# Optimization experiments

Measured on AMD Instinct MI355X. Metric: run time of the kernel, lower is better.

The kernel has to match this reference:

```python
import jax, jax.numpy as jnp
import numpy as np

N = 100_000      # n_nodes
E = 1_600_000    # n_edges (avg degree 16)
D_IN, D_H, D_OUT = 128, 128, 64
SIM_THRESH = 0.1


def setup_inputs() -> dict:
    key = jax.random.key(0)
    k = jax.random.split(key, 6)
    row = jax.random.randint(k[0], (E,), 0, N, dtype=jnp.int32)
    off = jax.random.randint(k[1], (E,), 1, N, dtype=jnp.int32)
    col = ((row + off) % N).astype(jnp.int32)  # guarantees no self-loops
    edge_index = jnp.stack([row, col], axis=0)
    x = jax.random.normal(k[2], (N, D_IN), dtype=jnp.float32)
    W1 = jax.random.normal(k[3], (D_IN, D_H), dtype=jnp.float32) / np.sqrt(D_IN)
    b1 = jnp.zeros((D_H,), jnp.float32)
    W2 = jax.random.normal(k[4], (D_H, D_OUT), dtype=jnp.float32) / np.sqrt(D_H)
    b2 = jnp.zeros((D_OUT,), jnp.float32)
    return {"x": x, "edge_index": edge_index, "W1": W1, "b1": b1, "W2": W2, "b2": b2}


def _att_coef(x, row, col, valid):
    """Edge-wise cosine-similarity attention (GNNGuard att_coef), fixed edge set.
    valid: bool [E] mask of edges still alive (pass-1 pruning).
    Returns per-edge weight w [E] (0 for pruned edges), per-node self-loop
    weight w_self [N], and the surviving-edge mask."""
    # cosine similarity per edge (never materialize NxN)
    xn = x / jnp.maximum(jnp.linalg.norm(x, axis=1, keepdims=True), 1e-12)
    sim = jnp.einsum('ed,ed->e', xn[row], xn[col])           # [E]
    sim = jnp.where(sim < SIM_THRESH, 0.0, sim)
    sim = jnp.where(valid, sim, 0.0)
    # L1 row normalization (segment reduce over destination rows)
    rowsum = jax.ops.segment_sum(sim, row, num_segments=N)   # [N]
    rs = rowsum[row]
    att = jnp.where(rs > 0, sim / jnp.where(rs > 0, rs, 1.0), 0.0)
    nz = att > 0                                             # edges kept by sparse matrix
    # degree-based self-loop weight: lam = 1/(deg+1)
    deg = jax.ops.segment_sum(nz.astype(x.dtype), row, num_segments=N)
    lam = 1.0 / (deg + 1.0)
    # exponentiate only stored (nonzero) entries, matching scipy sparse semantics
    w = jnp.where(nz, jnp.exp(att), 0.0)                     # [E]
    w_self = jnp.exp(lam)                                    # [N]
    return w, w_self, nz


def _gcn_conv(x, row, col, w, w_self, W, b):
    """GCNConv with given edge weights + self-loop weights, symmetric norm."""
    h = x @ W                                                # [N, d_out]
    deg = jax.ops.segment_sum(w, row, num_segments=N) + w_self
    dinv = jnp.where(deg > 0, jax.lax.rsqrt(deg), 0.0)       # deg^-1/2
    we = dinv[row] * w * dinv[col]                           # [E]
    agg = jax.ops.segment_sum(we[:, None] * h[col], row, num_segments=N)
    agg = agg + (w_self * dinv * dinv)[:, None] * h          # self-loop term
    return agg + b


def reference(x, edge_index, W1, b1, W2, b2):
    row, col = edge_index[0], edge_index[1]
    all_valid = jnp.ones((E,), dtype=bool)
    # attention pass 1 on raw features
    w1e, w1s, nz1 = _att_coef(x, row, col, all_valid)
    h = jax.nn.relu(_gcn_conv(x, row, col, w1e, w1s, W1, b1))
    # attention pass 2 on hidden features, restricted to surviving edges
    # (self-loops added in pass 1 are stripped again before re-normalization)
    w2e, w2s, _ = _att_coef(h, row, col, nz1)
    # dropout is identity at inference (training=False)
    out = _gcn_conv(h, row, col, w2e, w2s, W2, b2)
    return jax.nn.log_softmax(out, axis=1)
```

## Files before the change

kernel.cpp:

```cpp
#include <hip/hip_runtime.h>
#include <math.h>

#define SIM_THRESH 0.1f
#define Q_SCREEN_THRESH 0.085f

static __device__ __forceinline__ int dot4i8(int a, int b, int acc) {
#if __has_builtin(__builtin_amdgcn_sdot4)
  return __builtin_amdgcn_sdot4(a, b, acc, false);
#else
  const char4 av = *(const char4*)&a;
  const char4 bv = *(const char4*)&b;
  return acc + (int)av.x * bv.x + (int)av.y * bv.y + (int)av.z * bv.z + (int)av.w * bv.w;
#endif
}

__global__ void norms_q_kernel(const float* __restrict__ x, float* __restrict__ norm,
                               char* __restrict__ qn, int n) {
  int gid = blockIdx.x * blockDim.x + threadIdx.x;
  int r = gid >> 6, lane = gid & 63;
  if (r >= n) return;
  float2 v = ((const float2*)(x + (size_t)r * 128))[lane];
  float s = v.x * v.x + v.y * v.y;
#pragma unroll
  for (int o = 1; o < 64; o <<= 1) s += __shfl_xor(s, o);
  float nr = sqrtf(s);
  if (lane == 0) norm[r] = nr;
  float inv = 127.f / fmaxf(nr, 1e-12f);
  int qa = (int)rintf(v.x * inv);
  int qb = (int)rintf(v.y * inv);
  unsigned short packed = (unsigned short)((qa & 0xff) | ((qb & 0xff) << 8));
  *(unsigned short*)(qn + (size_t)r * 128 + lane * 2) = packed;
}

template <int DOUT>
__global__ void __launch_bounds__(256) gemm_kernel(const float* __restrict__ X,
                                                   const float* __restrict__ W,
                                                   float* __restrict__ out, int n) {
  constexpr int BM = 128, BK = 32;
  constexpr int TN = DOUT / 16;
  constexpr int XS = BK + 4;
  constexpr int WS = DOUT + 4;
  __shared__ float Xs[BM * XS];
  __shared__ float Ws[BK * WS];

  const int t = threadIdx.x;
  const int tx = t & 15;
  const int ty = t >> 4;
  const int base = blockIdx.x * BM;

  float acc[8][TN];
#pragma unroll
  for (int i = 0; i < 8; ++i)
#pragma unroll
    for (int j = 0; j < TN; ++j) acc[i][j] = 0.f;

  const int lr = t >> 3;
  const int lk4 = (t & 7) * 4;
  constexpr int F4R = DOUT / 4;
  constexpr int KSTEP = 256 / F4R;
  const int wc = t % F4R;
  const int wk0 = t / F4R;

  for (int kb = 0; kb < 128; kb += BK) {
    __syncthreads();
#pragma unroll
    for (int j = 0; j < 4; ++j) {
      int r = lr + 32 * j;
      int gr = base + r;
      float4 v = make_float4(0.f, 0.f, 0.f, 0.f);
      if (gr < n) v = *(const float4*)(X + (size_t)gr * 128 + kb + lk4);
      *(float4*)(Xs + r * XS + lk4) = v;
    }
#pragma unroll
    for (int k = wk0; k < BK; k += KSTEP) {
      float4 v = *(const float4*)(W + (size_t)(kb + k) * DOUT + wc * 4);
      *(float4*)(Ws + k * WS + wc * 4) = v;
    }
    __syncthreads();

#pragma unroll
    for (int k4 = 0; k4 < BK; k4 += 4) {
      float4 xf[8];
#pragma unroll
      for (int i = 0; i < 8; ++i) xf[i] = *(const float4*)(Xs + (ty + 16 * i) * XS + k4);
      float4 wf[4][TN / 4];
#pragma unroll
      for (int kk = 0; kk < 4; ++kk)
#pragma unroll
        for (int jj = 0; jj < TN / 4; ++jj)
          wf[kk][jj] = *(const float4*)(Ws + (k4 + kk) * WS + tx * TN + jj * 4);
#pragma unroll
      for (int i = 0; i < 8; ++i) {
        const float xk[4] = {xf[i].x, xf[i].y, xf[i].z, xf[i].w};
#pragma unroll
        for (int kk = 0; kk < 4; ++kk) {
#pragma unroll
          for (int jj = 0; jj < TN / 4; ++jj) {
            acc[i][jj * 4 + 0] = fmaf(xk[kk], wf[kk][jj].x, acc[i][jj * 4 + 0]);
            acc[i][jj * 4 + 1] = fmaf(xk[kk], wf[kk][jj].y, acc[i][jj * 4 + 1]);
            acc[i][jj * 4 + 2] = fmaf(xk[kk], wf[kk][jj].z, acc[i][jj * 4 + 2]);
            acc[i][jj * 4 + 3] = fmaf(xk[kk], wf[kk][jj].w, acc[i][jj * 4 + 3]);
          }
        }
      }
    }
  }

#pragma unroll
  for (int i = 0; i < 8; ++i) {
    int gr = base + ty + 16 * i;
    if (gr < n) {
#pragma unroll
      for (int jj = 0; jj < TN / 4; ++jj) {
        float4 v = make_float4(acc[i][jj * 4 + 0], acc[i][jj * 4 + 1], acc[i][jj * 4 + 2],
                               acc[i][jj * 4 + 3]);
        *(float4*)(out + (size_t)gr * DOUT + tx * TN + jj * 4) = v;
      }
    }
  }
}

__global__ void sim1_kernel(const char* __restrict__ qn, const float* __restrict__ x,
                            const float* __restrict__ norm, const int* __restrict__ row,
                            const int* __restrict__ col, float* __restrict__ sim,
                            int* __restrict__ cnt, int e) {
  int gid = blockIdx.x * blockDim.x + threadIdx.x;
  int p = gid >> 4, l = gid & 15;
  if (p >= e) return;
  int r = __builtin_nontemporal_load(row + p);
  int c = __builtin_nontemporal_load(col + p);
  int2 qa = *(const int2*)(qn + (size_t)r * 128 + l * 8);
  int2 qb = *(const int2*)(qn + (size_t)c * 128 + l * 8);
  int si = 0;
  si = dot4i8(qa.x, qb.x, si);
  si = dot4i8(qa.y, qb.y, si);
#pragma unroll
  for (int o = 1; o < 16; o <<= 1) si += __shfl_xor(si, o);
  float v = (float)si * (1.f / 16129.f);
  if (v > Q_SCREEN_THRESH) {
    const float4* fr = (const float4*)(x + (size_t)r * 128) + 2 * l;
    const float4* fc = (const float4*)(x + (size_t)c * 128) + 2 * l;
    float4 a0 = fr[0], a1 = fr[1], b0 = fc[0], b1 = fc[1];
    float t = a0.x * b0.x + a0.y * b0.y + a0.z * b0.z + a0.w * b0.w + a1.x * b1.x + a1.y * b1.y +
              a1.z * b1.z + a1.w * b1.w;
#pragma unroll
    for (int o = 1; o < 16; o <<= 1) t += __shfl_xor(t, o);
    float nr = fmaxf(norm[r], 1e-12f), nc = fmaxf(norm[c], 1e-12f);
    v = t / (nr * nc);
  } else {
    v = 0.f;
  }
  if (l == 0) {
    v = (v < SIM_THRESH) ? 0.f : v;
    __builtin_nontemporal_store(v, sim + p);
    if (v > 0.f) atomicAdd(&cnt[r], 1);
  }
}

__global__ void scan1_kernel(const int* __restrict__ cnt, int* __restrict__ excl,
                             int* __restrict__ bsum, int n) {
  __shared__ int sd[256];
  int t = threadIdx.x;
  int base = blockIdx.x * 1024 + t * 4;
  int v[4];
  int s = 0;
#pragma unroll
  for (int k = 0; k < 4; k++) {
    int idx = base + k;
    v[k] = (idx < n) ? cnt[idx] : 0;
    s += v[k];
  }
  sd[t] = s;
  __syncthreads();
  for (int off = 1; off < 256; off <<= 1) {
    int tmp = (t >= off) ? sd[t - off] : 0;
    __syncthreads();
    sd[t] += tmp;
    __syncthreads();
  }
  int ex = sd[t] - s;
#pragma unroll
  for (int k = 0; k < 4; k++) {
    int idx = base + k;
    if (idx < n) excl[idx] = ex;
    ex += v[k];
  }
  if (t == 255) bsum[blockIdx.x] = sd[255];
}

__global__ void scan2_kernel(int* __restrict__ bsum, int nb, int* __restrict__ total_out) {
  if (threadIdx.x == 0 && blockIdx.x == 0) {
    int acc = 0;
    for (int i = 0; i < nb; i++) {
      int v = bsum[i];
      bsum[i] = acc;
      acc += v;
    }
    *total_out = acc;
  }
}

__global__ void scan3_kernel(int* __restrict__ excl, const int* __restrict__ bsum, int n) {
  int i = blockIdx.x * 1024 + threadIdx.x;
  if (i < n) excl[i] += bsum[blockIdx.x];
}

__global__ void fillc_kernel(const int* __restrict__ row, const int* __restrict__ col,
                             const float* __restrict__ sim, const int* __restrict__ rp,
                             int* __restrict__ cur, int4* __restrict__ rec, int e) {
  int i = blockIdx.x * blockDim.x + threadIdx.x;
  if (i < e) {
    float s = __builtin_nontemporal_load(sim + i);
    if (s > 0.f) {
      int r = __builtin_nontemporal_load(row + i);
      int cc = __builtin_nontemporal_load(col + i);
      int p = rp[r] + atomicAdd(&cur[r], 1);
      int4 v;
      v.x = r;
      v.y = cc;
      v.z = __float_as_int(s);
      v.w = 0;
      rec[p] = v;
    }
  }
}

__global__ void row_att1_kernel(const int* __restrict__ rp, const int4* __restrict__ rec,
                                float* __restrict__ w, float* __restrict__ wself,
                                float* __restrict__ dinv, int n) {
  int r = blockIdx.x * blockDim.x + threadIdx.x;
  if (r >= n) return;
  int s0 = rp[r], s1 = rp[r + 1];
  float rs = 0.f;
  for (int p = s0; p < s1; p++) rs += __int_as_float(rec[p].z);
  float degw = 0.f;
  for (int p = s0; p < s1; p++) {
    float wv = expf(__int_as_float(rec[p].z) / rs);
    w[p] = wv;
    degw += wv;
  }
  float ws = expf(1.f / (float)(s1 - s0 + 1));
  degw += ws;
  wself[r] = ws;
  dinv[r] = 1.f / sqrtf(degw);
}

__global__ void agg_relu_norm_kernel(const float* __restrict__ hin, const int* __restrict__ rp,
                                     const int4* __restrict__ rec, const float* __restrict__ w,
                                     const float* __restrict__ wself,
                                     const float* __restrict__ dinv,
                                     const float* __restrict__ bias, float* __restrict__ hout,
                                     float* __restrict__ normout, int n) {
  int gid = blockIdx.x * blockDim.x + threadIdx.x;
  int r = gid >> 6, lane = gid & 63;
  if (r >= n) return;
  float di = dinv[r];
  float2 acc = {0.f, 0.f};
  int s0 = rp[r], s1 = rp[r + 1];
  for (int p = s0; p < s1; p++) {
    int c = rec[p].y;
    float we = di * w[p] * dinv[c];
    float2 hv = ((const float2*)(hin + (size_t)c * 128))[lane];
    acc.x = fmaf(we, hv.x, acc.x);
    acc.y = fmaf(we, hv.y, acc.y);
  }
  float self = wself[r] * di * di;
  float2 hr = ((const float2*)(hin + (size_t)r * 128))[lane];
  float2 bv = ((const float2*)bias)[lane];
  acc.x = fmaf(self, hr.x, acc.x) + bv.x;
  acc.y = fmaf(self, hr.y, acc.y) + bv.y;
  acc.x = fmaxf(acc.x, 0.f);
  acc.y = fmaxf(acc.y, 0.f);
  ((float2*)(hout + (size_t)r * 128))[lane] = acc;
  float s = acc.x * acc.x + acc.y * acc.y;
#pragma unroll
  for (int o = 1; o < 64; o <<= 1) s += __shfl_xor(s, o);
  if (lane == 0) normout[r] = sqrtf(s);
}

__global__ void sim2_kernel(const float* __restrict__ h, const float* __restrict__ norm,
                            const int4* __restrict__ rec, const int* __restrict__ nnz_p,
                            float* __restrict__ sim2) {
  int nnz = *nnz_p;
  int tid = blockIdx.x * blockDim.x + threadIdx.x;
  int ngroups = (gridDim.x * blockDim.x) >> 4;
  int g = tid >> 4, l = tid & 15;
  for (int p = g; p < nnz; p += ngroups) {
    int4 rv = rec[p];
    int r = rv.x, c = rv.y;
    const float4* fr = (const float4*)(h + (size_t)r * 128) + 2 * l;
    const float4* fc = (const float4*)(h + (size_t)c * 128) + 2 * l;
    float4 a0 = fr[0], a1 = fr[1], b0 = fc[0], b1 = fc[1];
    float s = a0.x * b0.x + a0.y * b0.y + a0.z * b0.z + a0.w * b0.w + a1.x * b1.x + a1.y * b1.y +
              a1.z * b1.z + a1.w * b1.w;
#pragma unroll
    for (int o = 1; o < 16; o <<= 1) s += __shfl_xor(s, o);
    if (l == 0) {
      float nr = fmaxf(norm[r], 1e-12f), nc = fmaxf(norm[c], 1e-12f);
      float v = s / (nr * nc);
      sim2[p] = (v < SIM_THRESH) ? 0.f : v;
    }
  }
}

__global__ void row_att2_kernel(const int* __restrict__ rp, const float* __restrict__ sim2,
                                float* __restrict__ w, float* __restrict__ wself,
                                float* __restrict__ dinv, int n) {
  int r = blockIdx.x * blockDim.x + threadIdx.x;
  if (r >= n) return;
  int s0 = rp[r], s1 = rp[r + 1];
  float rs = 0.f;
  int cnt2 = 0;
  for (int p = s0; p < s1; p++) {
    float sv = sim2[p];
    rs += sv;
    if (sv > 0.f) cnt2++;
  }
  float degw = 0.f;
  for (int p = s0; p < s1; p++) {
    float sv = sim2[p];
    float wv = (sv > 0.f) ? expf(sv / rs) : 0.f;
    w[p] = wv;
    degw += wv;
  }
  float ws = expf(1.f / (float)(cnt2 + 1));
  degw += ws;
  wself[r] = ws;
  dinv[r] = 1.f / sqrtf(degw);
}

__global__ void agg2_lsm_kernel(const float* __restrict__ hin, const int* __restrict__ rp,
                                const int4* __restrict__ rec, const float* __restrict__ w,
                                const float* __restrict__ wself, const float* __restrict__ dinv,
                                const float* __restrict__ bias, float* __restrict__ out, int n) {
  int gid = blockIdx.x * blockDim.x + threadIdx.x;
  int r = gid >> 6, lane = gid & 63;
  if (r >= n) return;
  float di = dinv[r];
  float acc = 0.f;
  int s0 = rp[r], s1 = rp[r + 1];
  for (int p = s0; p < s1; p++) {
    float wv = w[p];
    if (wv > 0.f) {
      int c = rec[p].y;
      acc = fmaf(di * wv * dinv[c], hin[(size_t)c * 64 + lane], acc);
    }
  }
  acc += wself[r] * di * di * hin[(size_t)r * 64 + lane] + bias[lane];
  float m = acc;
#pragma unroll
  for (int o = 1; o < 64; o <<= 1) m = fmaxf(m, __shfl_xor(m, o));
  float ex = expf(acc - m);
  float ssum = ex;
#pragma unroll
  for (int o = 1; o < 64; o <<= 1) ssum += __shfl_xor(ssum, o);
  out[(size_t)r * 64 + lane] = acc - m - logf(ssum);
}

extern "C" void kernel_launch(void* const* d_in, const int* in_sizes, int n_in, void* d_out,
                              int out_size, void* d_ws, size_t ws_size, hipStream_t stream) {
  const float* x = (const float*)d_in[0];
  const int* ei = (const int*)d_in[1];
  const float* W1 = (const float*)d_in[2];
  const float* b1 = (const float*)d_in[3];
  const float* W2 = (const float*)d_in[4];
  const float* b2 = (const float*)d_in[5];
  const int n = in_sizes[0] / 128;
  const int e = in_sizes[1] / 2;
  const int* row = ei;
  const int* col = ei + e;

  char* ws = (char*)d_ws;
  size_t off = 0;
  auto alloc = [&](size_t bytes) -> char* {
    char* p = ws + off;
    off = (off + bytes + 511) & ~(size_t)511;
    return p;
  };
  float* h1 = (float*)alloc((size_t)n * 128 * 4);
  float* h = (float*)alloc((size_t)n * 128 * 4);
  int4* rec = (int4*)alloc((size_t)e * 16);
  float* recf = (float*)rec;
  char* qn = (char*)rec;
  float* wbuf = recf + (size_t)2 * e;
  float* sim2b = recf + (size_t)3 * e;
  float* simb = h;
  int* rp = (int*)alloc((size_t)(n + 1) * 4);
  int* cnt = (int*)alloc((size_t)n * 4);
  int* cur = (int*)alloc((size_t)n * 4);
  float* norm = (float*)alloc((size_t)n * 4);
  float* wself = (float*)alloc((size_t)n * 4);
  float* dinv = (float*)alloc((size_t)n * 4);
  const int nb = (n + 1023) / 1024;
  int* bsum = (int*)alloc((size_t)nb * 4);
  float* h2 = h1;
  float* out = (float*)d_out;

  hipMemsetAsync(cnt, 0, (size_t)n * 4, stream);
  hipMemsetAsync(cur, 0, (size_t)n * 4, stream);

  const int gblocks = (n + 127) / 128;
  norms_q_kernel<<<(n * 64 + 255) / 256, 256, 0, stream>>>(x, norm, qn, n);
  gemm_kernel<128><<<gblocks, 256, 0, stream>>>(x, W1, h1, n);
  sim1_kernel<<<(e * 16 + 255) / 256, 256, 0, stream>>>(qn, x, norm, row, col, simb, cnt, e);
  scan1_kernel<<<nb, 256, 0, stream>>>(cnt, rp, bsum, n);
  scan2_kernel<<<1, 64, 0, stream>>>(bsum, nb, rp + n);
  scan3_kernel<<<nb, 1024, 0, stream>>>(rp, bsum, n);
  fillc_kernel<<<(e + 255) / 256, 256, 0, stream>>>(row, col, simb, rp, cur, rec, e);
  row_att1_kernel<<<(n + 255) / 256, 256, 0, stream>>>(rp, rec, wbuf, wself, dinv, n);
  agg_relu_norm_kernel<<<(n * 64 + 255) / 256, 256, 0, stream>>>(h1, rp, rec, wbuf, wself, dinv,
                                                                 b1, h, norm, n);
  sim2_kernel<<<4096, 256, 0, stream>>>(h, norm, rec, rp + n, sim2b);
  row_att2_kernel<<<(n + 255) / 256, 256, 0, stream>>>(rp, sim2b, wbuf, wself, dinv, n);
  gemm_kernel<64><<<gblocks, 256, 0, stream>>>(h, W2, h2, n);
  agg2_lsm_kernel<<<(n * 64 + 255) / 256, 256, 0, stream>>>(h2, rp, rec, wbuf, wself, dinv, b2,
                                                            out, n);
}
```

Before: 389.7 us.

## Bucket edges by destination row block before similarity and CSR fill

Adds a counting-sort pass that groups edges into buckets of 64 destination rows (count, scan, scatter) and feeds the bucketed row/col arrays to sim1 and fillc. The goal is locality: row features and the cnt/cur atomics are touched by nearby threads, which cuts scattered gathers and atomic contention. It costs three extra passes over the edge list plus atomics, and the serial scan2 is replaced by a single-block parallel scan. The bucket buffers alias the h buffer, which is not yet live at that point.

Result: slower. 860.3 us (+120.7%).

```diff
diff --git a/kernel.cpp b/kernel.cpp
--- a/kernel.cpp
+++ b/kernel.cpp
@@ -120,19 +120,63 @@
   }
 }
 
+__global__ void bcnt_kernel(const int* __restrict__ row, int* __restrict__ bcnt, int e) {
+  int i = blockIdx.x * blockDim.x + threadIdx.x;
+  if (i < e) atomicAdd(&bcnt[__builtin_nontemporal_load(row + i) >> 6], 1);
+}
+
+__global__ void small_scan_kernel(int* __restrict__ data, int m, int* __restrict__ total_out) {
+  __shared__ int sd[256];
+  __shared__ int carry;
+  int t = threadIdx.x;
+  if (t == 0) carry = 0;
+  __syncthreads();
+  for (int base = 0; base < m; base += 256) {
+    int idx = base + t;
+    int v = (idx < m) ? data[idx] : 0;
+    sd[t] = v;
+    __syncthreads();
+    for (int off = 1; off < 256; off <<= 1) {
+      int tmp = (t >= off) ? sd[t - off] : 0;
+      __syncthreads();
+      sd[t] += tmp;
+      __syncthreads();
+    }
+    int excl = sd[t] - v + carry;
+    if (idx < m) data[idx] = excl;
+    __syncthreads();
+    if (t == 255) carry += sd[255];
+    __syncthreads();
+  }
+  if (t == 0 && total_out) *total_out = carry;
+}
+
+__global__ void bscatter_kernel(const int* __restrict__ row, const int* __restrict__ col,
+                                const int* __restrict__ boff, int* __restrict__ bcur,
+                                int* __restrict__ brow, int* __restrict__ bcol, int e) {
+  int i = blockIdx.x * blockDim.x + threadIdx.x;
+  if (i < e) {
+    int r = __builtin_nontemporal_load(row + i);
+    int c = __builtin_nontemporal_load(col + i);
+    int b = r >> 6;
+    int pos = boff[b] + atomicAdd(&bcur[b], 1);
+    brow[pos] = r;
+    bcol[pos] = c;
+  }
+}
+
 __global__ void sim1_kernel(const char* __restrict__ qn, const float* __restrict__ x,
-                            const float* __restrict__ norm, const int* __restrict__ row,
-                            const int* __restrict__ col, float* __restrict__ sim,
+                            const float* __restrict__ norm, const int* __restrict__ brow,
+                            const int* __restrict__ bcol, float* __restrict__ sim,
                             int* __restrict__ cnt, int e) {
   int gid = blockIdx.x * blockDim.x + threadIdx.x;
   int p = gid >> 4, l = gid & 15;
   if (p >= e) return;
-  int r = __builtin_nontemporal_load(row + p);
-  int c = __builtin_nontemporal_load(col + p);
+  int r = brow[p];
+  int c = bcol[p];
   int2 qa = *(const int2*)(qn + (size_t)r * 128 + l * 8);
   int2 qb = *(const int2*)(qn + (size_t)c * 128 + l * 8);
-  int si = 0;
-  si = dot4i8(qa.x, qb.x, si);
+  int si = dot4i8(qa.x, qb.x, 0);
   si = dot4i8(qa.y, qb.y, si);
 #pragma unroll
   for (int o = 1; o < 16; o <<= 1) si += __shfl_xor(si, o);
@@ -152,7 +196,7 @@
   }
   if (l == 0) {
     v = (v < SIM_THRESH) ? 0.f : v;
-    __builtin_nontemporal_store(v, sim + p);
+    sim[p] = v;
     if (v > 0.f) atomicAdd(&cnt[r], 1);
   }
 }
@@ -188,32 +232,20 @@
   if (t == 255) bsum[blockIdx.x] = sd[255];
 }
 
-__global__ void scan2_kernel(int* __restrict__ bsum, int nb, int* __restrict__ total_out) {
-  if (threadIdx.x == 0 && blockIdx.x == 0) {
-    int acc = 0;
-    for (int i = 0; i < nb; i++) {
-      int v = bsum[i];
-      bsum[i] = acc;
-      acc += v;
-    }
-    *total_out = acc;
-  }
-}
-
 __global__ void scan3_kernel(int* __restrict__ excl, const int* __restrict__ bsum, int n) {
   int i = blockIdx.x * 1024 + threadIdx.x;
   if (i < n) excl[i] += bsum[blockIdx.x];
 }
 
-__global__ void fillc_kernel(const int* __restrict__ row, const int* __restrict__ col,
+__global__ void fillc_kernel(const int* __restrict__ brow, const int* __restrict__ bcol,
                              const float* __restrict__ sim, const int* __restrict__ rp,
                              int* __restrict__ cur, int4* __restrict__ rec, int e) {
   int i = blockIdx.x * blockDim.x + threadIdx.x;
   if (i < e) {
-    float s = __builtin_nontemporal_load(sim + i);
+    float s = sim[i];
     if (s > 0.f) {
-      int r = __builtin_nontemporal_load(row + i);
-      int cc = __builtin_nontemporal_load(col + i);
+      int r = brow[i];
+      int cc = bcol[i];
       int p = rp[r] + atomicAdd(&cur[r], 1);
       int4 v;
       v.x = r;
@@ -379,12 +411,14 @@
   };
   float* h1 = (float*)alloc((size_t)n * 128 * 4);
   float* h = (float*)alloc((size_t)n * 128 * 4);
+  float* simb = h;
+  int* brow = (int*)(h + (size_t)e);
+  int* bcol = (int*)(h + (size_t)2 * e);
   int4* rec = (int4*)alloc((size_t)e * 16);
   float* recf = (float*)rec;
   char* qn = (char*)rec;
   float* wbuf = recf + (size_t)2 * e;
   float* sim2b = recf + (size_t)3 * e;
-  float* simb = h;
   int* rp = (int*)alloc((size_t)(n + 1) * 4);
   int* cnt = (int*)alloc((size_t)n * 4);
   int* cur = (int*)alloc((size_t)n * 4);
@@ -393,20 +427,28 @@
   float* dinv = (float*)alloc((size_t)n * 4);
   const int nb = (n + 1023) / 1024;
   int* bsum = (int*)alloc((size_t)nb * 4);
+  const int nbuck = (n + 63) >> 6;
+  int* boff = (int*)alloc((size_t)nbuck * 4);
+  int* bcur = (int*)alloc((size_t)nbuck * 4);
   float* h2 = h1;
   float* out = (float*)d_out;
 
   hipMemsetAsync(cnt, 0, (size_t)n * 4, stream);
   hipMemsetAsync(cur, 0, (size_t)n * 4, stream);
+  hipMemsetAsync(boff, 0, (size_t)nbuck * 4, stream);
+  hipMemsetAsync(bcur, 0, (size_t)nbuck * 4, stream);
 
   const int gblocks = (n + 127) / 128;
   norms_q_kernel<<<(n * 64 + 255) / 256, 256, 0, stream>>>(x, norm, qn, n);
   gemm_kernel<128><<<gblocks, 256, 0, stream>>>(x, W1, h1, n);
-  sim1_kernel<<<(e * 16 + 255) / 256, 256, 0, stream>>>(qn, x, norm, row, col, simb, cnt, e);
+  bcnt_kernel<<<(e + 255) / 256, 256, 0, stream>>>(row, boff, e);
+  small_scan_kernel<<<1, 256, 0, stream>>>(boff, nbuck, nullptr);
+  bscatter_kernel<<<(e + 255) / 256, 256, 0, stream>>>(row, col, boff, bcur, brow, bcol, e);
+  sim1_kernel<<<(e * 16 + 255) / 256, 256, 0, stream>>>(qn, x, norm, brow, bcol, simb, cnt, e);
   scan1_kernel<<<nb, 256, 0, stream>>>(cnt, rp, bsum, n);
-  scan2_kernel<<<1, 64, 0, stream>>>(bsum, nb, rp + n);
+  small_scan_kernel<<<1, 256, 0, stream>>>(bsum, nb, rp + n);
   scan3_kernel<<<nb, 1024, 0, stream>>>(rp, bsum, n);
-  fillc_kernel<<<(e + 255) / 256, 256, 0, stream>>>(row, col, simb, rp, cur, rec, e);
+  fillc_kernel<<<(e + 255) / 256, 256, 0, stream>>>(brow, bcol, simb, rp, cur, rec, e);
   row_att1_kernel<<<(n + 255) / 256, 256, 0, stream>>>(rp, rec, wbuf, wself, dinv, n);
   agg_relu_norm_kernel<<<(n * 64 + 255) / 256, 256, 0, stream>>>(h1, rp, rec, wbuf, wself, dinv,
                                                                  b1, h, norm, n);
```
